# Kernel optimization log

Measured on AMD Instinct MI355X. Metric: run time of the kernel, lower is better.

Reference implementation:

```python
import jax, jax.numpy as jnp
import numpy as np
from jax.ops import segment_sum, segment_max

N_NODES = 50000
N_EDGES = 800000
B = 1024            # number of graphs
NODE_DIM = 21
ESM_DIM = 480
TAB_DIM = 7
H = 128             # hidden_dim
LSTM_H = H // 2     # 64 per direction
NEG_SLOPE = 0.2
BN_EPS = 1e-5


def setup_inputs() -> dict:
    key = jax.random.key(0)
    ks = iter(jax.random.split(key, 48))
    r = lambda shape, s=0.05: (s * jax.random.normal(next(ks), shape)).astype(jnp.float32)
    inp = {
        'x': jax.random.normal(next(ks), (N_NODES, NODE_DIM), dtype=jnp.float32),
        'edge_index': jax.random.randint(next(ks), (2, N_EDGES), 0, N_NODES, dtype=jnp.int64),
        'batch': jnp.sort(jax.random.randint(next(ks), (N_NODES,), 0, B, dtype=jnp.int64)),
        'esm_emb': jax.random.normal(next(ks), (B, ESM_DIM), dtype=jnp.float32),
        'tab_feats': jax.random.normal(next(ks), (B, TAB_DIM), dtype=jnp.float32),
        # GATConv 1 (heads=1)
        'gat1_W': r((H, NODE_DIM)), 'gat1_asrc': r((H,)), 'gat1_adst': r((H,)), 'gat1_b': r((H,)),
        # GATConv 2
        'gat2_W': r((H, H)), 'gat2_asrc': r((H,)), 'gat2_adst': r((H,)), 'gat2_b': r((H,)),
        # Bidirectional LSTM (seq_len=1, so a single cell step per direction)
        'lstm_Wih_f': r((4 * LSTM_H, ESM_DIM)), 'lstm_Whh_f': r((4 * LSTM_H, LSTM_H)),
        'lstm_bih_f': r((4 * LSTM_H,)), 'lstm_bhh_f': r((4 * LSTM_H,)),
        'lstm_Wih_r': r((4 * LSTM_H, ESM_DIM)), 'lstm_Whh_r': r((4 * LSTM_H, LSTM_H)),
        'lstm_bih_r': r((4 * LSTM_H,)), 'lstm_bhh_r': r((4 * LSTM_H,)),
        # tabular net
        'tab_W': r((64, TAB_DIM)), 'tab_b': r((64,)), 'tab_bn_g': jnp.ones((64,), jnp.float32), 'tab_bn_b': jnp.zeros((64,), jnp.float32),
        # fusion head
        'fus1_W': r((256, 320)), 'fus1_b': r((256,)), 'fus_bn_g': jnp.ones((256,), jnp.float32), 'fus_bn_b': jnp.zeros((256,), jnp.float32),
        'fus2_W': r((128, 256)), 'fus2_b': r((128,)),
        'fus3_W': r((1, 128)), 'fus3_b': r((1,)),
    }
    return inp


def _gat(h_in, src, dst, W, a_src, a_dst, bias):
    # PyG GATConv, heads=1, concat=True, self-loops already appended.
    h = h_in @ W.T                                  # [N, H]
    alpha_s = h @ a_src                             # [N]
    alpha_d = h @ a_dst                             # [N]
    e = jax.nn.leaky_relu(alpha_s[src] + alpha_d[dst], NEG_SLOPE)  # [E]
    m = segment_max(e, dst, num_segments=N_NODES)   # stable softmax per target
    ex = jnp.exp(e - m[dst])
    den = segment_sum(ex, dst, num_segments=N_NODES)
    coef = ex / (den[dst] + 1e-16)
    out = segment_sum(coef[:, None] * h[src], dst, num_segments=N_NODES)
    return out + bias


def _bn(x, g, b):
    # BatchNorm1d in training mode: biased batch statistics
    mu = jnp.mean(x, axis=0)
    var = jnp.var(x, axis=0)
    return (x - mu) * jax.lax.rsqrt(var + BN_EPS) * g + b


def _lstm_step(x, Wih, Whh, bih, bhh):
    # single step with zero initial (h, c); Whh term vanishes but kept for fidelity
    g = x @ Wih.T + bih + jnp.zeros((x.shape[0], Whh.shape[1]), x.dtype) @ Whh.T + bhh
    i, f, gg, o = jnp.split(g, 4, axis=1)           # PyTorch gate order i,f,g,o
    c = jax.nn.sigmoid(i) * jnp.tanh(gg)
    return jax.nn.sigmoid(o) * jnp.tanh(c)


def reference(x, edge_index, batch, esm_emb, tab_feats,
              gat1_W, gat1_asrc, gat1_adst, gat1_b,
              gat2_W, gat2_asrc, gat2_adst, gat2_b,
              lstm_Wih_f, lstm_Whh_f, lstm_bih_f, lstm_bhh_f,
              lstm_Wih_r, lstm_Whh_r, lstm_bih_r, lstm_bhh_r,
              tab_W, tab_b, tab_bn_g, tab_bn_b,
              fus1_W, fus1_b, fus_bn_g, fus_bn_b,
              fus2_W, fus2_b, fus3_W, fus3_b):
    sl = jnp.arange(N_NODES, dtype=edge_index.dtype)
    src = jnp.concatenate([edge_index[0], sl])      # add_self_loops=True default
    dst = jnp.concatenate([edge_index[1], sl])

    h1 = jax.nn.relu(_gat(x, src, dst, gat1_W, gat1_asrc, gat1_adst, gat1_b))
    h2 = jax.nn.relu(_gat(h1, src, dst, gat2_W, gat2_asrc, gat2_adst, gat2_b))

    counts = segment_sum(jnp.ones((N_NODES,), h2.dtype), batch, num_segments=B)
    graph_embed = segment_sum(h2, batch, num_segments=B) / jnp.maximum(counts, 1.0)[:, None]

    # bilstm over seq_len=1: output at last (only) step = concat(fwd, bwd)
    h_f = _lstm_step(esm_emb, lstm_Wih_f, lstm_Whh_f, lstm_bih_f, lstm_bhh_f)
    h_r = _lstm_step(esm_emb, lstm_Wih_r, lstm_Whh_r, lstm_bih_r, lstm_bhh_r)
    seq_embed = jnp.concatenate([h_f, h_r], axis=1)  # [B, 128]

    tab_embed = jax.nn.relu(_bn(tab_feats @ tab_W.T + tab_b, tab_bn_g, tab_bn_b))

    z = jnp.concatenate([graph_embed, seq_embed, tab_embed], axis=1)  # [B, 320]
    z = jax.nn.relu(_bn(z @ fus1_W.T + fus1_b, fus_bn_g, fus_bn_b))   # dropout: identity (eval)
    z = jax.nn.relu(z @ fus2_W.T + fus2_b)
    return z @ fus3_W.T + fus3_b                     # [B, 1]
```

## Files before the change

### kernel.cpp

```cpp
#include <hip/hip_runtime.h>
#include <hip/hip_bf16.h>

#define N_NODES 50000
#define N_PAD   50048
#define N_EDGES 800000
#define E_TOT   850000
#define NB      1024
#define ESM_DIM 480
#define HD      128
#define NBUCK   196
#define CAP     5120
#define EPB     3321
#define SC_BLK  256
#define CVT_BLK 256
#define BND_BLK 196
#define WC_BLK  16
#define TAB_BLK 4
#define G1B     782
#define LSTM_B  96
#define LG      384
#define AGG_GRID 12500
#define NL_BLK  512

typedef short short8 __attribute__((ext_vector_type(8)));
typedef unsigned short ushort8 __attribute__((ext_vector_type(8)));
typedef float f32x4 __attribute__((ext_vector_type(4)));

__device__ __forceinline__ float bf2f(unsigned int u) {
    union { unsigned int i; float f; } c; c.i = u << 16; return c.f;
}
__device__ __forceinline__ unsigned short f2bf(float f) {
    union { float f; unsigned int i; } c; c.f = f;
    unsigned int i = c.i;
    return (unsigned short)((i + 0x7FFFu + ((i >> 16) & 1u)) >> 16);
}
__device__ __forceinline__ void split2(float v, unsigned short& h, unsigned short& l) {
    h = f2bf(v);
    l = f2bf(v - bf2f(h));
}


__device__ void dev_scatter(const int* __restrict__ ei, int* __restrict__ gcur,
                            int* __restrict__ pairs, int blk) {
    __shared__ int hist[NBUCK];
    int t = threadIdx.x;
    for (int u = t; u < NBUCK; u += 256) hist[u] = 0;
    __syncthreads();
    int e0 = blk * EPB;
    int e1 = (e0 + EPB < E_TOT) ? e0 + EPB : E_TOT;
    for (int e = e0 + t; e < e1; e += 256) {
        int d = (e < N_EDGES) ? ei[N_EDGES + e] : (e - N_EDGES);
        atomicAdd(&hist[d >> 8], 1);
    }
    __syncthreads();
    for (int u = t; u < NBUCK; u += 256) {
        int c = hist[u];
        hist[u] = (c > 0) ? atomicAdd(&gcur[u], c) : 0;
    }
    __syncthreads();
    for (int e = e0 + t; e < e1; e += 256) {
        int s, d;
        if (e < N_EDGES) { s = ei[e]; d = ei[N_EDGES + e]; }
        else             { s = d = e - N_EDGES; }
        int bu = d >> 8;
        int pos = atomicAdd(&hist[bu], 1);
        pairs[bu * CAP + pos] = s | ((d & 255) << 16);
    }
}

__device__ void dev_cvt(const float* __restrict__ esm,
                        const float* __restrict__ Wf,
                        const float* __restrict__ Wr,
                        const float* __restrict__ W1,
                        unsigned short* __restrict__ esm_h, unsigned short* __restrict__ esm_l,
                        unsigned short* __restrict__ wg_h,  unsigned short* __restrict__ wg_l,
                        unsigned short* __restrict__ w1h,   unsigned short* __restrict__ w1l,
                        int blk) {
    int tid = blk * 256 + threadIdx.x;
    for (int u = tid; u < NB * 120; u += CVT_BLK * 256) {
        float4 v = ((const float4*)esm)[u];
        ushort4 h, l;
        split2(v.x, h.x, l.x); split2(v.y, h.y, l.y);
        split2(v.z, h.z, l.z); split2(v.w, h.w, l.w);
        ((ushort4*)esm_h)[u] = h; ((ushort4*)esm_l)[u] = l;
    }
    for (int u = tid; u < LG * 120; u += CVT_BLK * 256) {
        int n = u / 120, kk = u - n * 120;
        int rr = (n >= 192) ? n - 192 : n;
        const float* Ws = (n >= 192) ? Wr : Wf;
        int srow = (rr < 64) ? rr : rr + 64;
        float4 v = *(const float4*)&Ws[(size_t)srow * 480 + kk * 4];
        ushort4 h, l;
        split2(v.x, h.x, l.x); split2(v.y, h.y, l.y);
        split2(v.z, h.z, l.z); split2(v.w, h.w, l.w);
        ((ushort4*)wg_h)[u] = h; ((ushort4*)wg_l)[u] = l;
    }
    for (int u = tid; u < 128 * 32; u += CVT_BLK * 256) {
        int f = u >> 5, k = u & 31;
        float v = (k < 21) ? W1[f * 21 + k] : 0.f;
        unsigned short h, l;
        split2(v, h, l);
        w1h[u] = h; w1l[u] = l;
    }
}

__device__ void dev_tab4(const float* __restrict__ tf, const float* __restrict__ W,
                         const float* __restrict__ bias, const float* __restrict__ g,
                         const float* __restrict__ b, float* __restrict__ z, int blk) {
    __shared__ float ssum[16][16];
    __shared__ float ssq[16][16];
    int t = threadIdx.x;
    int rg = t >> 4, jl = t & 15;
    int j = blk * 16 + jl;
    float Wj[7];
#pragma unroll
    for (int k = 0; k < 7; ++k) Wj[k] = W[j * 7 + k];
    float bj = bias[j];
    float s = 0.f, q = 0.f;
    for (int rr = 0; rr < 64; ++rr) {
        int row = rg * 64 + rr;
        const float* xp = &tf[(size_t)row * 7];
        float a = bj;
#pragma unroll
        for (int k = 0; k < 7; ++k) a += xp[k] * Wj[k];
        s += a; q += a * a;
    }
    ssum[rg][jl] = s; ssq[rg][jl] = q;
    __syncthreads();
    for (int off = 8; off; off >>= 1) {
        if (rg < off) { ssum[rg][jl] += ssum[rg + off][jl]; ssq[rg][jl] += ssq[rg + off][jl]; }
        __syncthreads();
    }
    float mu = ssum[0][jl] * (1.f / 1024.f);
    float var = ssq[0][jl] * (1.f / 1024.f) - mu * mu;
    float sc = rsqrtf(var + 1e-5f) * g[j];
    float sh = b[j] - mu * sc;
    for (int rr = 0; rr < 64; ++rr) {
        int row = rg * 64 + rr;
        const float* xp = &tf[(size_t)row * 7];
        float a = bj;
#pragma unroll
        for (int k = 0; k < 7; ++k) a += xp[k] * Wj[k];
        z[(size_t)row * 320 + 256 + j] = fmaxf(a * sc + sh, 0.f);
    }
}

__global__ __launch_bounds__(256) void megaA(
        const int* __restrict__ ei, int* __restrict__ gcur, int* __restrict__ pairs,
        const float* __restrict__ esm, const float* __restrict__ Wih_f,
        const float* __restrict__ Wih_r, const float* __restrict__ gat1_W,
        unsigned short* __restrict__ esm_h, unsigned short* __restrict__ esm_l,
        unsigned short* __restrict__ wg_h,  unsigned short* __restrict__ wg_l,
        unsigned short* __restrict__ w1h,   unsigned short* __restrict__ w1l,
        const int* __restrict__ batch, int* __restrict__ gstart,
        const float* __restrict__ W2, unsigned short* __restrict__ Wb,
        const float* __restrict__ tf, const float* __restrict__ tab_W,
        const float* __restrict__ tab_b, const float* __restrict__ tab_g,
        const float* __restrict__ tab_bb, float* __restrict__ z) {
    int b = blockIdx.x, t = threadIdx.x;
    if (b < SC_BLK) {
        dev_scatter(ei, gcur, pairs, b);
    } else if (b < SC_BLK + CVT_BLK) {
        dev_cvt(esm, Wih_f, Wih_r, gat1_W, esm_h, esm_l, wg_h, wg_l, w1h, w1l, b - SC_BLK);
    } else if (b < SC_BLK + CVT_BLK + BND_BLK) {
        int i = (b - (SC_BLK + CVT_BLK)) * 256 + t;
        if (i >= N_NODES) return;
        int bb = batch[i];
        int bp = (i == 0) ? -1 : batch[i - 1];
        for (int g = bp + 1; g <= bb; ++g) gstart[g] = i;
        if (i == N_NODES - 1)
            for (int g = bb + 1; g <= NB; ++g) gstart[g] = N_NODES;
    } else if (b < SC_BLK + CVT_BLK + BND_BLK + WC_BLK) {
        int i = (b - (SC_BLK + CVT_BLK + BND_BLK)) * 256 + t;
        if (i >= 128 * 32) return;
        float4 v = ((const float4*)W2)[i];
        ((ushort4*)Wb)[i] = make_ushort4(f2bf(v.x), f2bf(v.y), f2bf(v.z), f2bf(v.w));
    } else {
        dev_tab4(tf, tab_W, tab_b, tab_g, tab_bb, z,
                 b - (SC_BLK + CVT_BLK + BND_BLK + WC_BLK));
    }
}


__device__ __forceinline__ float sigmoidf_(float x) { return 1.f / (1.f + __expf(-x)); }

__device__ void dev_gat1_mfma(const float* __restrict__ X,
                              const unsigned short* __restrict__ w1h,
                              const unsigned short* __restrict__ w1l,
                              const float* __restrict__ asrc, const float* __restrict__ adst,
                              unsigned short* __restrict__ out,
                              float* __restrict__ alpha_s, float* __restrict__ alpha_d,
                              int blk) {
    int t = threadIdx.x;
    int wid = t >> 6, L = t & 63, quad = L >> 4, lo = L & 15;
    int m0 = blk * 64 + wid * 16;
    int row = m0 + lo;
    const float* xr = X + (size_t)row * 21;
    int kbase = quad * 8;
    bool valid = row < N_NODES;
    float xv[8];
#pragma unroll
    for (int j = 0; j < 8; ++j) {
        int k = kbase + j;
        xv[j] = (valid && k < 21) ? xr[k] : 0.f;
    }
    short8 ah, al;
#pragma unroll
    for (int j = 0; j < 8; ++j) {
        unsigned short h, l;
        split2(xv[j], h, l);
        ah[j] = (short)h; al[j] = (short)l;
    }
    float as_p[4] = {0.f, 0.f, 0.f, 0.f};
    float ad_p[4] = {0.f, 0.f, 0.f, 0.f};
#pragma unroll
    for (int ft = 0; ft < 8; ++ft) {
        short8 bh = *(const short8*)&w1h[(ft * 16 + lo) * 32 + kbase];
        short8 bl = *(const short8*)&w1l[(ft * 16 + lo) * 32 + kbase];
        f32x4 acc = {0.f, 0.f, 0.f, 0.f};
        acc = __builtin_amdgcn_mfma_f32_16x16x32_bf16(ah, bh, acc, 0, 0, 0);
        acc = __builtin_amdgcn_mfma_f32_16x16x32_bf16(al, bh, acc, 0, 0, 0);
        acc = __builtin_amdgcn_mfma_f32_16x16x32_bf16(ah, bl, acc, 0, 0, 0);
        float asv = asrc[ft * 16 + lo];
        float adv = adst[ft * 16 + lo];
#pragma unroll
        for (int r = 0; r < 4; ++r) {
            int m = m0 + quad * 4 + r;
            out[(size_t)m * HD + ft * 16 + lo] = f2bf(acc[r]);
            as_p[r] += acc[r] * asv;
            ad_p[r] += acc[r] * adv;
        }
    }
#pragma unroll
    for (int off = 1; off < 16; off <<= 1) {
#pragma unroll
        for (int r = 0; r < 4; ++r) {
            as_p[r] += __shfl_xor(as_p[r], off);
            ad_p[r] += __shfl_xor(ad_p[r], off);
        }
    }
    if (lo == 0) {
#pragma unroll
        for (int r = 0; r < 4; ++r) {
            int m = m0 + quad * 4 + r;
            if (m < N_NODES) { alpha_s[m] = as_p[r]; alpha_d[m] = ad_p[r]; }
        }
    }
}

__device__ void dev_lstm_mfma(const unsigned short* __restrict__ Ah,
                              const unsigned short* __restrict__ Al,
                              const unsigned short* __restrict__ Bh,
                              const unsigned short* __restrict__ Bl,
                              float* __restrict__ G, int blk) {
    __shared__ unsigned short Bsh[64][104];
    __shared__ unsigned short Bsl[64][104];
    int t = threadIdx.x;
    int wid = t >> 6, L = t & 63, quad = L >> 4, lo = L & 15;
    int nt = blk % 6, mt = blk / 6;
    int m0 = mt * 64 + wid * 16;
    int n0 = nt * 64;
    f32x4 accs[4];
#pragma unroll
    for (int ft = 0; ft < 4; ++ft) accs[ft] = (f32x4){0.f, 0.f, 0.f, 0.f};
    const unsigned short* arh = Ah + (size_t)(m0 + lo) * ESM_DIM;
    const unsigned short* arl = Al + (size_t)(m0 + lo) * ESM_DIM;
    for (int c = 0; c < 5; ++c) {
        int k0c = c * 96;
        short8 ah[3], al[3];
#pragma unroll
        for (int ks = 0; ks < 3; ++ks) {
            ah[ks] = *(const short8*)&arh[k0c + ks * 32 + quad * 8];
            al[ks] = *(const short8*)&arl[k0c + ks * 32 + quad * 8];
        }
#pragma unroll
        for (int u = 0; u < 3; ++u) {
            int li = u * 2048 + t * 8;
            int row = li / 96, col = li % 96;
            *(ushort8*)&Bsh[row][col] =
                *(const ushort8*)&Bh[(size_t)(n0 + row) * ESM_DIM + k0c + col];
            *(ushort8*)&Bsl[row][col] =
                *(const ushort8*)&Bl[(size_t)(n0 + row) * ESM_DIM + k0c + col];
        }
        __syncthreads();
#pragma unroll
        for (int ks = 0; ks < 3; ++ks) {
#pragma unroll
            for (int ft = 0; ft < 4; ++ft) {
                short8 bh = *(const short8*)&Bsh[ft * 16 + lo][ks * 32 + quad * 8];
                short8 bl = *(const short8*)&Bsl[ft * 16 + lo][ks * 32 + quad * 8];
                accs[ft] = __builtin_amdgcn_mfma_f32_16x16x32_bf16(ah[ks], bh, accs[ft], 0, 0, 0);
                accs[ft] = __builtin_amdgcn_mfma_f32_16x16x32_bf16(al[ks], bh, accs[ft], 0, 0, 0);
                accs[ft] = __builtin_amdgcn_mfma_f32_16x16x32_bf16(ah[ks], bl, accs[ft], 0, 0, 0);
            }
        }
        __syncthreads();
    }
#pragma unroll
    for (int ft = 0; ft < 4; ++ft) {
#pragma unroll
        for (int r = 0; r < 4; ++r)
            G[(size_t)(m0 + quad * 4 + r) * LG + n0 + ft * 16 + lo] = accs[ft][r];
    }
}

__global__ __launch_bounds__(256) void megaB(
        const int* __restrict__ gcur, const int* __restrict__ pairs,
        int* __restrict__ row_beg, int* __restrict__ row_end, int* __restrict__ csr_src,
        const float* __restrict__ x,
        const unsigned short* __restrict__ w1h, const unsigned short* __restrict__ w1l,
        const float* __restrict__ gat1_as, const float* __restrict__ gat1_ad,
        unsigned short* __restrict__ h0, float* __restrict__ alpha_s, float* __restrict__ alpha_d,
        const unsigned short* __restrict__ esm_h, const unsigned short* __restrict__ esm_l,
        const unsigned short* __restrict__ wg_h,  const unsigned short* __restrict__ wg_l,
        float* __restrict__ g_lstm) {
    int b = blockIdx.x, t = threadIdx.x;
    if (b < NBUCK) {
        __shared__ int dc[256];
        __shared__ int wt[4];
        __shared__ int cur[256];
        int rs = b * CAP;
        int re = rs + gcur[b];
        dc[t] = 0;
        __syncthreads();
        for (int i = rs + t; i < re; i += 1024) {
            int i1 = i + 256, i2 = i + 512, i3 = i + 768;
            int p0 = pairs[i];
            int p1 = (i1 < re) ? pairs[i1] : 0;
            int p2 = (i2 < re) ? pairs[i2] : 0;
            int p3 = (i3 < re) ? pairs[i3] : 0;
            atomicAdd(&dc[p0 >> 16], 1);
            if (i1 < re) atomicAdd(&dc[p1 >> 16], 1);
            if (i2 < re) atomicAdd(&dc[p2 >> 16], 1);
            if (i3 < re) atomicAdd(&dc[p3 >> 16], 1);
        }
        __syncthreads();
        int v = dc[t];
        int lane = t & 63, wid = t >> 6;
        int sc = v;
#pragma unroll
        for (int off = 1; off < 64; off <<= 1) {
            int n = __shfl_up(sc, off);
            if (lane >= off) sc += n;
        }
        if (lane == 63) wt[wid] = sc;
        __syncthreads();
        int pref = 0;
        for (int ww = 0; ww < wid; ++ww) pref += wt[ww];
        int beg = rs + pref + sc - v;
        int node = b * 256 + t;
        if (node < N_NODES) { row_beg[node] = beg; row_end[node] = beg + v; }
        cur[t] = beg;
        __syncthreads();
        for (int i = rs + t; i < re; i += 1024) {
            int i1 = i + 256, i2 = i + 512, i3 = i + 768;
            int p0 = pairs[i];
            int p1 = (i1 < re) ? pairs[i1] : 0;
            int p2 = (i2 < re) ? pairs[i2] : 0;
            int p3 = (i3 < re) ? pairs[i3] : 0;
            int pos0 = atomicAdd(&cur[p0 >> 16], 1);
            csr_src[pos0] = p0 & 0xFFFF;
            if (i1 < re) { int pos = atomicAdd(&cur[p1 >> 16], 1); csr_src[pos] = p1 & 0xFFFF; }
            if (i2 < re) { int pos = atomicAdd(&cur[p2 >> 16], 1); csr_src[pos] = p2 & 0xFFFF; }
            if (i3 < re) { int pos = atomicAdd(&cur[p3 >> 16], 1); csr_src[pos] = p3 & 0xFFFF; }
        }
    } else if (b < NBUCK + LSTM_B) {
        dev_lstm_mfma(esm_h, esm_l, wg_h, wg_l, g_lstm, b - NBUCK);
    } else {
        dev_gat1_mfma(x, w1h, w1l, gat1_as, gat1_ad, h0, alpha_s, alpha_d,
                      b - (NBUCK + LSTM_B));
    }
}


__global__ __launch_bounds__(256) void gemm_mfma(const unsigned short* __restrict__ A,
                                                 const unsigned short* __restrict__ Wb,
                                                 const float* __restrict__ asrc,
                                                 const float* __restrict__ adst,
                                                 unsigned short* __restrict__ out,
                                                 float* __restrict__ alpha_s,
                                                 float* __restrict__ alpha_d, int M) {
    __shared__ unsigned short Wlds[128 * 136];
    int t = threadIdx.x;
    for (int u = t; u < 128 * 16; u += 256) {
        int row = u >> 4, seg = u & 15;
        *(ushort8*)&Wlds[row * 136 + seg * 8] = *(const ushort8*)&Wb[row * 128 + seg * 8];
    }
    __syncthreads();
    int wid = t >> 6, L = t & 63;
    int quad = L >> 4, lo = L & 15;
    int m0 = blockIdx.x * 64 + wid * 16;
    short8 afrag[4];
#pragma unroll
    for (int ch = 0; ch < 4; ++ch)
        afrag[ch] = *(const short8*)&A[(size_t)(m0 + lo) * HD + ch * 32 + quad * 8];
    float as_p[4] = {0.f, 0.f, 0.f, 0.f};
    float ad_p[4] = {0.f, 0.f, 0.f, 0.f};
#pragma unroll
    for (int ft = 0; ft < 8; ++ft) {
        f32x4 acc = {0.f, 0.f, 0.f, 0.f};
#pragma unroll
        for (int ch = 0; ch < 4; ++ch) {
            short8 b = *(const short8*)&Wlds[(ft * 16 + lo) * 136 + ch * 32 + quad * 8];
            acc = __builtin_amdgcn_mfma_f32_16x16x32_bf16(afrag[ch], b, acc, 0, 0, 0);
        }
        float asv = asrc[ft * 16 + lo];
        float adv = adst[ft * 16 + lo];
#pragma unroll
        for (int r = 0; r < 4; ++r) {
            int m = m0 + quad * 4 + r;
            if (m < M) out[(size_t)m * HD + ft * 16 + lo] = f2bf(acc[r]);
            as_p[r] += acc[r] * asv;
            ad_p[r] += acc[r] * adv;
        }
    }
#pragma unroll
    for (int off = 1; off < 16; off <<= 1) {
#pragma unroll
        for (int r = 0; r < 4; ++r) {
            as_p[r] += __shfl_xor(as_p[r], off);
            ad_p[r] += __shfl_xor(ad_p[r], off);
        }
    }
    if (lo == 0) {
#pragma unroll
        for (int r = 0; r < 4; ++r) {
            int m = m0 + quad * 4 + r;
            if (m < M) { alpha_s[m] = as_p[r]; alpha_d[m] = ad_p[r]; }
        }
    }
}


__global__ void gat_spmm(const unsigned short* __restrict__ h, const int* __restrict__ row_beg,
                         const int* __restrict__ row_end, const int* __restrict__ csr_src,
                         const float* __restrict__ alpha_s, const float* __restrict__ alpha_d,
                         const float* __restrict__ bias, unsigned short* __restrict__ outp,
                         const float* __restrict__ g_lstm,
                         const float* __restrict__ bihf, const float* __restrict__ bhhf,
                         const float* __restrict__ bihr, const float* __restrict__ bhhr,
                         float* __restrict__ z) {
    if (blockIdx.x >= AGG_GRID) {
        int idx = (blockIdx.x - AGG_GRID) * 256 + threadIdx.x;
        int bb = idx >> 7, jj = idx & 127;
        int dir = jj >> 6, j = jj & 63;
        const float* gb = g_lstm + (size_t)bb * LG + dir * 192;
        const float* bi = dir ? bihr : bihf;
        const float* bh = dir ? bhhr : bhhf;
        float gi = gb[j]        + bi[j]        + bh[j];
        float gg = gb[64 + j]   + bi[128 + j]  + bh[128 + j];
        float go = gb[128 + j]  + bi[192 + j]  + bh[192 + j];
        float c = sigmoidf_(gi) * tanhf(gg);
        z[(size_t)bb * 320 + 128 + jj] = sigmoidf_(go) * tanhf(c);
        return;
    }
    int w = (int)((blockIdx.x * (size_t)blockDim.x + threadIdx.x) >> 6);
    int lane = threadIdx.x & 63;
    if (w >= N_NODES) return;
    int grp = lane >> 4, l16 = lane & 15;
    int rs = row_beg[w], re = row_end[w];
    int deg = re - rs;
    float ad = alpha_d[w];
    float acc[8] = {0.f, 0.f, 0.f, 0.f, 0.f, 0.f, 0.f, 0.f};
    if (deg <= 64) {
        int s_reg = 0;
        float e = -1e30f;
        if (lane < deg) {
            s_reg = csr_src[rs + lane];
            float t0 = alpha_s[s_reg] + ad;
            e = (t0 > 0.f) ? t0 : 0.2f * t0;
        }
        float m = e;
#pragma unroll
        for (int off = 32; off; off >>= 1) m = fmaxf(m, __shfl_xor(m, off));
        float ex = (lane < deg) ? __expf(e - m) : 0.f;
        float den = ex;
#pragma unroll
        for (int off = 32; off; off >>= 1) den += __shfl_xor(den, off);
        float coef = ex / (den + 1e-16f);
        int i = rs + grp;
        for (; i + 4 < re; i += 8) {
            int idx = i - rs;
            float c0 = __shfl(coef, idx);
            int   s0 = __shfl(s_reg, idx);
            float c1 = __shfl(coef, idx + 4);
            int   s1 = __shfl(s_reg, idx + 4);
            ushort8 h0 = *(const ushort8*)&h[(size_t)s0 * HD + l16 * 8];
            ushort8 h1 = *(const ushort8*)&h[(size_t)s1 * HD + l16 * 8];
#pragma unroll
            for (int j = 0; j < 8; ++j) acc[j] += c0 * bf2f(h0[j]);
#pragma unroll
            for (int j = 0; j < 8; ++j) acc[j] += c1 * bf2f(h1[j]);
        }
        if (i < re) {
            int idx = i - rs;
            float c0 = __shfl(coef, idx);
            int   s0 = __shfl(s_reg, idx);
            ushort8 h0 = *(const ushort8*)&h[(size_t)s0 * HD + l16 * 8];
#pragma unroll
            for (int j = 0; j < 8; ++j) acc[j] += c0 * bf2f(h0[j]);
        }
    } else {
        float m = -1e30f;
        for (int i = rs + lane; i < re; i += 64) {
            int s = csr_src[i];
            float t0 = alpha_s[s] + ad;
            t0 = (t0 > 0.f) ? t0 : 0.2f * t0;
            m = fmaxf(m, t0);
        }
#pragma unroll
        for (int off = 32; off; off >>= 1) m = fmaxf(m, __shfl_xor(m, off));
        float den = 0.f;
        for (int i = rs + lane; i < re; i += 64) {
            int s = csr_src[i];
            float t0 = alpha_s[s] + ad;
            t0 = (t0 > 0.f) ? t0 : 0.2f * t0;
            den += __expf(t0 - m);
        }
#pragma unroll
        for (int off = 32; off; off >>= 1) den += __shfl_xor(den, off);
        float inv = 1.f / (den + 1e-16f);
        for (int i = rs + grp; i < re; i += 4) {
            int s = csr_src[i];
            float t0 = alpha_s[s] + ad;
            t0 = (t0 > 0.f) ? t0 : 0.2f * t0;
            float c = __expf(t0 - m) * inv;
            ushort8 hv = *(const ushort8*)&h[(size_t)s * HD + l16 * 8];
#pragma unroll
            for (int j = 0; j < 8; ++j) acc[j] += c * bf2f(hv[j]);
        }
    }
#pragma unroll
    for (int j = 0; j < 8; ++j) {
        acc[j] += __shfl_xor(acc[j], 16);
        acc[j] += __shfl_xor(acc[j], 32);
    }
    int f0 = l16 * 8 + grp * 2;
    float2 bv = *(const float2*)&bias[f0];
    float vx = fmaxf(acc[grp * 2]     + bv.x, 0.f);
    float vy = fmaxf(acc[grp * 2 + 1] + bv.y, 0.f);
    unsigned int pv = (unsigned int)f2bf(vx) | ((unsigned int)f2bf(vy) << 16);
    *(unsigned int*)&outp[(size_t)w * HD + f0] = pv;
}


__global__ void pool_kernel(const unsigned short* __restrict__ h, const int* __restrict__ start,
                            float* __restrict__ z) {
    int w = (int)((blockIdx.x * (size_t)blockDim.x + threadIdx.x) >> 6);
    int lane = threadIdx.x & 63;
    if (w >= NB) return;
    int grp = lane >> 4, l16 = lane & 15;
    int s0 = start[w], s1 = start[w + 1];
    float acc[8] = {0.f, 0.f, 0.f, 0.f, 0.f, 0.f, 0.f, 0.f};
    int n = s0 + grp;
    for (; n + 4 < s1; n += 8) {
        ushort8 a = *(const ushort8*)&h[(size_t)n * HD + l16 * 8];
        ushort8 b = *(const ushort8*)&h[(size_t)(n + 4) * HD + l16 * 8];
#pragma unroll
        for (int j = 0; j < 8; ++j) acc[j] += bf2f(a[j]);
#pragma unroll
        for (int j = 0; j < 8; ++j) acc[j] += bf2f(b[j]);
    }
    if (n < s1) {
        ushort8 a = *(const ushort8*)&h[(size_t)n * HD + l16 * 8];
#pragma unroll
        for (int j = 0; j < 8; ++j) acc[j] += bf2f(a[j]);
    }
#pragma unroll
    for (int j = 0; j < 8; ++j) {
        acc[j] += __shfl_xor(acc[j], 16);
        acc[j] += __shfl_xor(acc[j], 32);
    }
    float inv = 1.f / fmaxf((float)(s1 - s0), 1.f);
    int f0 = l16 * 8 + grp * 2;
    *(float2*)&z[(size_t)w * 320 + f0] =
        make_float2(acc[grp * 2] * inv, acc[grp * 2 + 1] * inv);
}


__global__ __launch_bounds__(256) void fus1_stats(const float* __restrict__ X,
                                                  const float* __restrict__ W1,
                                                  float* __restrict__ out,
                                                  float* __restrict__ colsum,
                                                  float* __restrict__ colsq) {
    __shared__ float Xs[16][33];
    __shared__ float Ws[64][33];
    __shared__ float cs[4][64];
    __shared__ float cq[4][64];
    int t = threadIdx.x;
    int r0 = blockIdx.x * 16;
    int fb = blockIdx.y * 64;
    const float* W = W1 + (size_t)fb * 320;
    int f = t & 63, rsub = t >> 6;
    float acc0 = 0.f, acc1 = 0.f, acc2 = 0.f, acc3 = 0.f;
    for (int kc = 0; kc < 320; kc += 32) {
        {
            int idx = t * 2, xr = idx >> 5, xk = idx & 31;
            const float2 v = *(const float2*)&X[(size_t)(r0 + xr) * 320 + kc + xk];
            Xs[xr][xk] = v.x; Xs[xr][xk + 1] = v.y;
        }
        {
            int wf = t >> 2, wk = (t & 3) * 8;
            const float4* p = (const float4*)&W[(size_t)wf * 320 + kc + wk];
            float4 a = p[0], b = p[1];
            Ws[wf][wk] = a.x; Ws[wf][wk + 1] = a.y; Ws[wf][wk + 2] = a.z; Ws[wf][wk + 3] = a.w;
            Ws[wf][wk + 4] = b.x; Ws[wf][wk + 5] = b.y; Ws[wf][wk + 6] = b.z; Ws[wf][wk + 7] = b.w;
        }
        __syncthreads();
#pragma unroll
        for (int k = 0; k < 32; ++k) {
            float w = Ws[f][k];
            acc0 += Xs[rsub][k] * w;
            acc1 += Xs[rsub + 4][k] * w;
            acc2 += Xs[rsub + 8][k] * w;
            acc3 += Xs[rsub + 12][k] * w;
        }
        __syncthreads();
    }
    out[(size_t)(r0 + rsub) * 256 + fb + f] = acc0;
    out[(size_t)(r0 + rsub + 4) * 256 + fb + f] = acc1;
    out[(size_t)(r0 + rsub + 8) * 256 + fb + f] = acc2;
    out[(size_t)(r0 + rsub + 12) * 256 + fb + f] = acc3;
    cs[rsub][f] = acc0 + acc1 + acc2 + acc3;
    cq[rsub][f] = acc0 * acc0 + acc1 * acc1 + acc2 * acc2 + acc3 * acc3;
    __syncthreads();
    if (rsub == 0) {
        atomicAdd(&colsum[fb + f], cs[0][f] + cs[1][f] + cs[2][f] + cs[3][f]);
        atomicAdd(&colsq[fb + f],  cq[0][f] + cq[1][f] + cq[2][f] + cq[3][f]);
    }
}


__global__ __launch_bounds__(256) void fus2_final(const float* __restrict__ z1pre,
                                                  const float* __restrict__ colsum,
                                                  const float* __restrict__ colsq,
                                                  const float* __restrict__ fus_g,
                                                  const float* __restrict__ fus_bb,
                                                  const float* __restrict__ W2,
                                                  const float* __restrict__ b2,
                                                  const float* __restrict__ W3,
                                                  const float* __restrict__ b3,
                                                  float* __restrict__ out) {
    __shared__ float Xs[16][33];
    __shared__ float Ws[128][33];
    __shared__ float rowsum[16];
    __shared__ float sc_[256], sh_[256];
    int t = threadIdx.x;
    {
        float mu = colsum[t] * (1.f / 1024.f);
        float var = colsq[t] * (1.f / 1024.f) - mu * mu;
        float s = rsqrtf(var + 1e-5f) * fus_g[t];
        sc_[t] = s;
        sh_[t] = fus_bb[t] - mu * s;
    }
    __syncthreads();
    int r0 = blockIdx.x * 16;
    int f = t & 127, rh = t >> 7;
    float acc[8] = {0.f, 0.f, 0.f, 0.f, 0.f, 0.f, 0.f, 0.f};
    for (int kc = 0; kc < 256; kc += 32) {
        {
            int idx = t * 2, xr = idx >> 5, xk = idx & 31;
            float2 v = *(const float2*)&z1pre[(size_t)(r0 + xr) * 256 + kc + xk];
            Xs[xr][xk]     = fmaxf(v.x * sc_[kc + xk]     + sh_[kc + xk], 0.f);
            Xs[xr][xk + 1] = fmaxf(v.y * sc_[kc + xk + 1] + sh_[kc + xk + 1], 0.f);
        }
#pragma unroll
        for (int i = 0; i < 4; ++i) {
            int id2 = t + 256 * i;
            int wf = id2 >> 3, wk = (id2 & 7) * 4;
            *(float4*)&Ws[wf][wk] = *(const float4*)&W2[(size_t)wf * 256 + kc + wk];
        }
        __syncthreads();
#pragma unroll
        for (int k = 0; k < 32; ++k) {
            float w = Ws[f][k];
#pragma unroll
            for (int r = 0; r < 8; ++r) acc[r] += Xs[rh * 8 + r][k] * w;
        }
        __syncthreads();
    }
    float bv = b2[f], wv = W3[f];
    if (t < 16) rowsum[t] = 0.f;
    __syncthreads();
#pragma unroll
    for (int r = 0; r < 8; ++r) {
        float v = fmaxf(acc[r] + bv, 0.f) * wv;
#pragma unroll
        for (int off = 32; off; off >>= 1) v += __shfl_xor(v, off);
        if ((t & 63) == 0) atomicAdd(&rowsum[rh * 8 + r], v);
    }
    __syncthreads();
    if (t < 16) out[r0 + t] = rowsum[t] + b3[0];
}


extern "C" void kernel_launch(void* const* d_in, const int* in_sizes, int n_in,
                              void* d_out, int out_size, void* d_ws, size_t ws_size,
                              hipStream_t stream) {
    const float* x        = (const float*)d_in[0];
    const int*   ei       = (const int*)d_in[1];
    const int*   batch    = (const int*)d_in[2];
    const float* esm      = (const float*)d_in[3];
    const float* tabf     = (const float*)d_in[4];
    const float* gat1_W   = (const float*)d_in[5];
    const float* gat1_as  = (const float*)d_in[6];
    const float* gat1_ad  = (const float*)d_in[7];
    const float* gat1_b   = (const float*)d_in[8];
    const float* gat2_W   = (const float*)d_in[9];
    const float* gat2_as  = (const float*)d_in[10];
    const float* gat2_ad  = (const float*)d_in[11];
    const float* gat2_b   = (const float*)d_in[12];
    const float* Wih_f    = (const float*)d_in[13];
    const float* bih_f    = (const float*)d_in[15];
    const float* bhh_f    = (const float*)d_in[16];
    const float* Wih_r    = (const float*)d_in[17];
    const float* bih_r    = (const float*)d_in[19];
    const float* bhh_r    = (const float*)d_in[20];
    const float* tab_W    = (const float*)d_in[21];
    const float* tab_b    = (const float*)d_in[22];
    const float* tab_g    = (const float*)d_in[23];
    const float* tab_bb   = (const float*)d_in[24];
    const float* fus1_W   = (const float*)d_in[25];
    const float* fus_g    = (const float*)d_in[27];
    const float* fus_bb   = (const float*)d_in[28];
    const float* fus2_W   = (const float*)d_in[29];
    const float* fus2_b   = (const float*)d_in[30];
    const float* fus3_W   = (const float*)d_in[31];
    const float* fus3_b   = (const float*)d_in[32];
    float* out = (float*)d_out;

    char* ws = (char*)d_ws;
    size_t off = 0;
    auto alloc = [&](size_t bytes) -> char* {
        char* p = ws + off;
        off += (bytes + 255) & ~(size_t)255;
        return p;
    };
    unsigned short* h0_bf = (unsigned short*)alloc((size_t)N_PAD * HD * 2);
    unsigned short* hA_bf = (unsigned short*)alloc((size_t)N_PAD * HD * 2);
    unsigned short* h2_bf = (unsigned short*)alloc((size_t)N_PAD * HD * 2);
    unsigned short* h_act = (unsigned short*)alloc((size_t)N_NODES * HD * 2);
    float* alpha_s = (float*)alloc((size_t)N_NODES * 4);
    float* alpha_d = (float*)alloc((size_t)N_NODES * 4);
    unsigned short* w2bf = (unsigned short*)alloc((size_t)HD * HD * 2);
    int*   row_beg = (int*)alloc((size_t)N_NODES * 4);
    int*   row_end = (int*)alloc((size_t)N_NODES * 4);
    int*   csr_src = (int*)alloc((size_t)NBUCK * CAP * 4);
    int*   pairs   = (int*)alloc((size_t)NBUCK * CAP * 4);
    int*   gstart  = (int*)alloc((size_t)(NB + 1) * 4);
    float* z1pre   = (float*)alloc((size_t)NB * 256 * 4);
    float* z       = (float*)alloc((size_t)NB * 320 * 4);
    float* g_lstm  = (float*)alloc((size_t)NB * LG * 4);
    unsigned short* esm_h = (unsigned short*)alloc((size_t)NB * ESM_DIM * 2);
    unsigned short* esm_l = (unsigned short*)alloc((size_t)NB * ESM_DIM * 2);
    unsigned short* wg_h  = (unsigned short*)alloc((size_t)LG * ESM_DIM * 2);
    unsigned short* wg_l  = (unsigned short*)alloc((size_t)LG * ESM_DIM * 2);
    unsigned short* w1h   = (unsigned short*)alloc((size_t)128 * 32 * 2);
    unsigned short* w1l   = (unsigned short*)alloc((size_t)128 * 32 * 2);
    int*   gcur    = (int*)alloc((size_t)NBUCK * 4);
    float* colsum  = (float*)alloc((size_t)256 * 4);
    float* colsq   = (float*)alloc((size_t)256 * 4);
    size_t zero_len = (size_t)((char*)colsq + 256 * 4 - (char*)gcur);
    hipMemsetAsync(gcur, 0, zero_len, stream);

    megaA<<<SC_BLK + CVT_BLK + BND_BLK + WC_BLK + TAB_BLK, 256, 0, stream>>>(
        ei, gcur, pairs, esm, Wih_f, Wih_r, gat1_W,
        esm_h, esm_l, wg_h, wg_l, w1h, w1l,
        batch, gstart, gat2_W, w2bf,
        tabf, tab_W, tab_b, tab_g, tab_bb, z);

    megaB<<<NBUCK + LSTM_B + G1B, 256, 0, stream>>>(
        gcur, pairs, row_beg, row_end, csr_src,
        x, w1h, w1l, gat1_as, gat1_ad, h0_bf, alpha_s, alpha_d,
        esm_h, esm_l, wg_h, wg_l, g_lstm);

    gat_spmm<<<AGG_GRID + NL_BLK, 256, 0, stream>>>(h0_bf, row_beg, row_end, csr_src,
                                                    alpha_s, alpha_d, gat1_b, hA_bf,
                                                    g_lstm, bih_f, bhh_f, bih_r, bhh_r, z);

    gemm_mfma<<<N_PAD / 64, 256, 0, stream>>>(hA_bf, w2bf, gat2_as, gat2_ad,
                                              h2_bf, alpha_s, alpha_d, N_NODES);

    gat_spmm<<<AGG_GRID, 256, 0, stream>>>(h2_bf, row_beg, row_end, csr_src,
                                           alpha_s, alpha_d, gat2_b, h_act,
                                           g_lstm, bih_f, bhh_f, bih_r, bhh_r, z);

    pool_kernel<<<(NB + 3) / 4, 256, 0, stream>>>(h_act, gstart, z);

    fus1_stats<<<dim3(64, 4), 256, 0, stream>>>(z, fus1_W, z1pre, colsum, colsq);

    fus2_final<<<64, 256, 0, stream>>>(z1pre, colsum, colsq, fus_g, fus_bb,
                                       fus2_W, fus2_b, fus3_W, fus3_b, out);

    (void)in_sizes; (void)n_in; (void)out_size; (void)ws_size;
}
```

Before: 292.3 us.

## Move fusion-head GEMMs to split-bf16 MFMA with three-product fp32 emulation

Rewrites the fus1 and fus2 dense layers to use 16x16x32 bf16 MFMA instructions in place of scalar fp32 FMA loops. Each fp32 value is split into high and low bf16 parts, and three MFMA products approximate fp32 accuracy. The change also switches to 64-row block tiles, which cuts the grid from 256 to 64 blocks and from 64 to 16. These GEMMs are small, so the fewer blocks give less parallelism and the per-chunk bf16 conversion adds overhead.

```diff
diff --git a/kernel.cpp b/kernel.cpp
--- a/kernel.cpp
+++ b/kernel.cpp
@@ -578,72 +578,100 @@
 }
 
 
-__global__ __launch_bounds__(256) void fus1_stats(const float* __restrict__ X,
-                                                  const float* __restrict__ W1,
-                                                  float* __restrict__ out,
-                                                  float* __restrict__ colsum,
-                                                  float* __restrict__ colsq) {
-    __shared__ float Xs[16][33];
-    __shared__ float Ws[64][33];
-    __shared__ float cs[4][64];
-    __shared__ float cq[4][64];
+__global__ __launch_bounds__(256) void fus1_mfma(const float* __restrict__ X,
+                                                 const float* __restrict__ W1,
+                                                 float* __restrict__ out,
+                                                 float* __restrict__ colsum,
+                                                 float* __restrict__ colsq) {
+    __shared__ unsigned short Bsh[64][72];
+    __shared__ unsigned short Bsl[64][72];
+    __shared__ float cls[64], clq[64];
     int t = threadIdx.x;
-    int r0 = blockIdx.x * 16;
-    int fb = blockIdx.y * 64;
-    const float* W = W1 + (size_t)fb * 320;
-    int f = t & 63, rsub = t >> 6;
-    float acc0 = 0.f, acc1 = 0.f, acc2 = 0.f, acc3 = 0.f;
-    for (int kc = 0; kc < 320; kc += 32) {
-        {
-            int idx = t * 2, xr = idx >> 5, xk = idx & 31;
-            const float2 v = *(const float2*)&X[(size_t)(r0 + xr) * 320 + kc + xk];
-            Xs[xr][xk] = v.x; Xs[xr][xk + 1] = v.y;
-        }
-        {
-            int wf = t >> 2, wk = (t & 3) * 8;
-            const float4* p = (const float4*)&W[(size_t)wf * 320 + kc + wk];
-            float4 a = p[0], b = p[1];
-            Ws[wf][wk] = a.x; Ws[wf][wk + 1] = a.y; Ws[wf][wk + 2] = a.z; Ws[wf][wk + 3] = a.w;
-            Ws[wf][wk + 4] = b.x; Ws[wf][wk + 5] = b.y; Ws[wf][wk + 6] = b.z; Ws[wf][wk + 7] = b.w;
-        }
-        __syncthreads();
-#pragma unroll
-        for (int k = 0; k < 32; ++k) {
-            float w = Ws[f][k];
-            acc0 += Xs[rsub][k] * w;
-            acc1 += Xs[rsub + 4][k] * w;
-            acc2 += Xs[rsub + 8][k] * w;
-            acc3 += Xs[rsub + 12][k] * w;
-        }
-        __syncthreads();
-    }
-    out[(size_t)(r0 + rsub) * 256 + fb + f] = acc0;
-    out[(size_t)(r0 + rsub + 4) * 256 + fb + f] = acc1;
-    out[(size_t)(r0 + rsub + 8) * 256 + fb + f] = acc2;
-    out[(size_t)(r0 + rsub + 12) * 256 + fb + f] = acc3;
-    cs[rsub][f] = acc0 + acc1 + acc2 + acc3;
-    cq[rsub][f] = acc0 * acc0 + acc1 * acc1 + acc2 * acc2 + acc3 * acc3;
+    int wid = t >> 6, L = t & 63, quad = L >> 4, lo = L & 15;
+    int m0 = blockIdx.x * 64 + wid * 16;
+    int n0 = blockIdx.y * 64;
+    if (t < 64) { cls[t] = 0.f; clq[t] = 0.f; }
+    f32x4 accs[4];
+#pragma unroll
+    for (int ft = 0; ft < 4; ++ft) accs[ft] = (f32x4){0.f, 0.f, 0.f, 0.f};
+    const float* ar = X + (size_t)(m0 + lo) * 320;
+    for (int c = 0; c < 5; ++c) {
+        int k0 = c * 64;
+        short8 ah[2], al[2];
+#pragma unroll
+        for (int ks = 0; ks < 2; ++ks) {
+            const float* ap = &ar[k0 + ks * 32 + quad * 8];
+            float4 v0 = *(const float4*)ap;
+            float4 v1 = *(const float4*)(ap + 4);
+            float av[8] = {v0.x, v0.y, v0.z, v0.w, v1.x, v1.y, v1.z, v1.w};
+#pragma unroll
+            for (int j = 0; j < 8; ++j) {
+                unsigned short hh, ll;
+                split2(av[j], hh, ll);
+                ah[ks][j] = (short)hh; al[ks][j] = (short)ll;
+            }
+        }
+#pragma unroll
+        for (int u = 0; u < 4; ++u) {
+            int li = u * 256 + t;
+            int row = li >> 4, col = (li & 15) * 4;
+            float4 v = *(const float4*)&W1[(size_t)(n0 + row) * 320 + k0 + col];
+            ushort4 hh, ll;
+            split2(v.x, hh.x, ll.x); split2(v.y, hh.y, ll.y);
+            split2(v.z, hh.z, ll.z); split2(v.w, hh.w, ll.w);
+            *(ushort4*)&Bsh[row][col] = hh;
+            *(ushort4*)&Bsl[row][col] = ll;
+        }
+        __syncthreads();
+#pragma unroll
+        for (int ks = 0; ks < 2; ++ks) {
+#pragma unroll
+            for (int ft = 0; ft < 4; ++ft) {
+                short8 bh = *(const short8*)&Bsh[ft * 16 + lo][ks * 32 + quad * 8];
+                short8 bl = *(const short8*)&Bsl[ft * 16 + lo][ks * 32 + quad * 8];
+                accs[ft] = __builtin_amdgcn_mfma_f32_16x16x32_bf16(ah[ks], bh, accs[ft], 0, 0, 0);
+                accs[ft] = __builtin_amdgcn_mfma_f32_16x16x32_bf16(al[ks], bh, accs[ft], 0, 0, 0);
+                accs[ft] = __builtin_amdgcn_mfma_f32_16x16x32_bf16(ah[ks], bl, accs[ft], 0, 0, 0);
+            }
+        }
+        __syncthreads();
+    }
+#pragma unroll
+    for (int ft = 0; ft < 4; ++ft) {
+        float s = 0.f, q = 0.f;
+#pragma unroll
+        for (int r = 0; r < 4; ++r) {
+            float v = accs[ft][r];
+            out[(size_t)(m0 + quad * 4 + r) * 256 + n0 + ft * 16 + lo] = v;
+            s += v; q += v * v;
+        }
+        s += __shfl_xor(s, 16); s += __shfl_xor(s, 32);
+        q += __shfl_xor(q, 16); q += __shfl_xor(q, 32);
+        if (quad == 0) {
+            atomicAdd(&cls[ft * 16 + lo], s);
+            atomicAdd(&clq[ft * 16 + lo], q);
+        }
+    }
     __syncthreads();
-    if (rsub == 0) {
-        atomicAdd(&colsum[fb + f], cs[0][f] + cs[1][f] + cs[2][f] + cs[3][f]);
-        atomicAdd(&colsq[fb + f],  cq[0][f] + cq[1][f] + cq[2][f] + cq[3][f]);
-    }
-}
-
-
-__global__ __launch_bounds__(256) void fus2_final(const float* __restrict__ z1pre,
-                                                  const float* __restrict__ colsum,
-                                                  const float* __restrict__ colsq,
-                                                  const float* __restrict__ fus_g,
-                                                  const float* __restrict__ fus_bb,
-                                                  const float* __restrict__ W2,
-                                                  const float* __restrict__ b2,
-                                                  const float* __restrict__ W3,
-                                                  const float* __restrict__ b3,
-                                                  float* __restrict__ out) {
-    __shared__ float Xs[16][33];
-    __shared__ float Ws[128][33];
-    __shared__ float rowsum[16];
+    if (t < 64) {
+        atomicAdd(&colsum[n0 + t], cls[t]);
+        atomicAdd(&colsq[n0 + t],  clq[t]);
+    }
+}
+
+
+__global__ __launch_bounds__(256) void fus2_mfma(const float* __restrict__ z1pre,
+                                                 const float* __restrict__ colsum,
+                                                 const float* __restrict__ colsq,
+                                                 const float* __restrict__ fus_g,
+                                                 const float* __restrict__ fus_bb,
+                                                 const float* __restrict__ W2,
+                                                 const float* __restrict__ b2,
+                                                 const float* __restrict__ W3,
+                                                 const float* __restrict__ b3,
+                                                 float* __restrict__ out) {
+    __shared__ unsigned short Bsh[128][72];
+    __shared__ unsigned short Bsl[128][72];
     __shared__ float sc_[256], sh_[256];
     int t = threadIdx.x;
     {
@@ -654,43 +682,74 @@
         sh_[t] = fus_bb[t] - mu * s;
     }
     __syncthreads();
-    int r0 = blockIdx.x * 16;
-    int f = t & 127, rh = t >> 7;
-    float acc[8] = {0.f, 0.f, 0.f, 0.f, 0.f, 0.f, 0.f, 0.f};
-    for (int kc = 0; kc < 256; kc += 32) {
-        {
-            int idx = t * 2, xr = idx >> 5, xk = idx & 31;
-            float2 v = *(const float2*)&z1pre[(size_t)(r0 + xr) * 256 + kc + xk];
-            Xs[xr][xk]     = fmaxf(v.x * sc_[kc + xk]     + sh_[kc + xk], 0.f);
-            Xs[xr][xk + 1] = fmaxf(v.y * sc_[kc + xk + 1] + sh_[kc + xk + 1], 0.f);
-        }
-#pragma unroll
-        for (int i = 0; i < 4; ++i) {
-            int id2 = t + 256 * i;
-            int wf = id2 >> 3, wk = (id2 & 7) * 4;
-            *(float4*)&Ws[wf][wk] = *(const float4*)&W2[(size_t)wf * 256 + kc + wk];
-        }
-        __syncthreads();
-#pragma unroll
-        for (int k = 0; k < 32; ++k) {
-            float w = Ws[f][k];
-#pragma unroll
-            for (int r = 0; r < 8; ++r) acc[r] += Xs[rh * 8 + r][k] * w;
-        }
-        __syncthreads();
-    }
-    float bv = b2[f], wv = W3[f];
-    if (t < 16) rowsum[t] = 0.f;
-    __syncthreads();
-#pragma unroll
-    for (int r = 0; r < 8; ++r) {
-        float v = fmaxf(acc[r] + bv, 0.f) * wv;
-#pragma unroll
-        for (int off = 32; off; off >>= 1) v += __shfl_xor(v, off);
-        if ((t & 63) == 0) atomicAdd(&rowsum[rh * 8 + r], v);
-    }
-    __syncthreads();
-    if (t < 16) out[r0 + t] = rowsum[t] + b3[0];
+    int wid = t >> 6, L = t & 63, quad = L >> 4, lo = L & 15;
+    int m0 = blockIdx.x * 64 + wid * 16;
+    f32x4 accs[8];
+#pragma unroll
+    for (int ft = 0; ft < 8; ++ft) accs[ft] = (f32x4){0.f, 0.f, 0.f, 0.f};
+    const float* ar = z1pre + (size_t)(m0 + lo) * 256;
+    for (int c = 0; c < 4; ++c) {
+        int k0 = c * 64;
+        short8 ah[2], al[2];
+#pragma unroll
+        for (int ks = 0; ks < 2; ++ks) {
+            int kb = k0 + ks * 32 + quad * 8;
+            float4 v0 = *(const float4*)&ar[kb];
+            float4 v1 = *(const float4*)&ar[kb + 4];
+            float av[8] = {v0.x, v0.y, v0.z, v0.w, v1.x, v1.y, v1.z, v1.w};
+#pragma unroll
+            for (int j = 0; j < 8; ++j) {
+                float xv = fmaxf(av[j] * sc_[kb + j] + sh_[kb + j], 0.f);
+                unsigned short hh, ll;
+                split2(xv, hh, ll);
+                ah[ks][j] = (short)hh; al[ks][j] = (short)ll;
+            }
+        }
+#pragma unroll
+        for (int u = 0; u < 8; ++u) {
+            int li = u * 256 + t;
+            int row = li >> 4, col = (li & 15) * 4;
+            float4 v = *(const float4*)&W2[(size_t)row * 256 + k0 + col];
+            ushort4 hh, ll;
+            split2(v.x, hh.x, ll.x); split2(v.y, hh.y, ll.y);
+            split2(v.z, hh.z, ll.z); split2(v.w, hh.w, ll.w);
+            *(ushort4*)&Bsh[row][col] = hh;
+            *(ushort4*)&Bsl[row][col] = ll;
+        }
+        __syncthreads();
+#pragma unroll
+        for (int ks = 0; ks < 2; ++ks) {
+#pragma unroll
+            for (int ft = 0; ft < 8; ++ft) {
+                short8 bh = *(const short8*)&Bsh[ft * 16 + lo][ks * 32 + quad * 8];
+                short8 bl = *(const short8*)&Bsl[ft * 16 + lo][ks * 32 + quad * 8];
+                accs[ft] = __builtin_amdgcn_mfma_f32_16x16x32_bf16(ah[ks], bh, accs[ft], 0, 0, 0);
+                accs[ft] = __builtin_amdgcn_mfma_f32_16x16x32_bf16(al[ks], bh, accs[ft], 0, 0, 0);
+                accs[ft] = __builtin_amdgcn_mfma_f32_16x16x32_bf16(ah[ks], bl, accs[ft], 0, 0, 0);
+            }
+        }
+        __syncthreads();
+    }
+    float b3v = b3[0];
+    float b2v[8], w3v[8];
+#pragma unroll
+    for (int ft = 0; ft < 8; ++ft) {
+        int col = ft * 16 + lo;
+        b2v[ft] = b2[col];
+        w3v[ft] = W3[col];
+    }
+#pragma unroll
+    for (int r = 0; r < 4; ++r) {
+        float rsum = 0.f;
+#pragma unroll
+        for (int ft = 0; ft < 8; ++ft)
+            rsum += fmaxf(accs[ft][r] + b2v[ft], 0.f) * w3v[ft];
+        rsum += __shfl_xor(rsum, 1);
+        rsum += __shfl_xor(rsum, 2);
+        rsum += __shfl_xor(rsum, 4);
+        rsum += __shfl_xor(rsum, 8);
+        if (lo == 0) out[m0 + quad * 4 + r] = rsum + b3v;
+    }
 }
 
 
@@ -787,10 +846,10 @@
 
     pool_kernel<<<(NB + 3) / 4, 256, 0, stream>>>(h_act, gstart, z);
 
-    fus1_stats<<<dim3(64, 4), 256, 0, stream>>>(z, fus1_W, z1pre, colsum, colsq);
-
-    fus2_final<<<64, 256, 0, stream>>>(z1pre, colsum, colsq, fus_g, fus_bb,
-                                       fus2_W, fus2_b, fus3_W, fus3_b, out);
+    fus1_mfma<<<dim3(16, 4), 256, 0, stream>>>(z, fus1_W, z1pre, colsum, colsq);
+
+    fus2_mfma<<<16, 256, 0, stream>>>(z1pre, colsum, colsq, fus_g, fus_bb,
+                                      fus2_W, fus2_b, fus3_W, fus3_b, out);
 
     (void)in_sizes; (void)n_in; (void)out_size; (void)ws_size;
 }
```

New measurement: 270.5 us (median of 2 runs). 7.5% less time.
